# Optimization experiments

Measured on AMD Instinct MI355X. Metric: run time of the kernel, lower is better.

The kernel has to match this reference:

```python
import jax, jax.numpy as jnp
import numpy as np

NUM_HEADS = 32
NUM_KV_HEADS = 8
HEAD_DIM = 128
HIDDEN = 4096
BASE = 10000.0


def setup_inputs() -> dict:
    key = jax.random.key(0)
    ks = jax.random.split(key, 9)
    bs, seq = 1, 2048
    x = jax.random.normal(ks[0], (bs, seq, HIDDEN), dtype=jnp.float32)
    position_ids = jnp.broadcast_to(jnp.arange(seq, dtype=jnp.int32), (bs, seq))
    s = 1.0 / np.sqrt(HIDDEN)
    wq = jax.random.normal(ks[1], (NUM_HEADS * HEAD_DIM, HIDDEN), dtype=jnp.float32) * s
    bq = jnp.zeros((NUM_HEADS * HEAD_DIM,), dtype=jnp.float32)
    wk = jax.random.normal(ks[2], (NUM_KV_HEADS * HEAD_DIM, HIDDEN), dtype=jnp.float32) * s
    bk = jnp.zeros((NUM_KV_HEADS * HEAD_DIM,), dtype=jnp.float32)
    wv = jax.random.normal(ks[3], (NUM_KV_HEADS * HEAD_DIM, HIDDEN), dtype=jnp.float32) * s
    bv = jnp.zeros((NUM_KV_HEADS * HEAD_DIM,), dtype=jnp.float32)
    wo = jax.random.normal(ks[4], (HIDDEN, NUM_HEADS * HEAD_DIM), dtype=jnp.float32) * s
    bo = jnp.zeros((HIDDEN,), dtype=jnp.float32)
    return {"x": x, "position_ids": position_ids, "wq": wq, "bq": bq,
            "wk": wk, "bk": bk, "wv": wv, "bv": bv, "wo": wo, "bo": bo}


def _rotate_half(t):
    h = t.shape[-1] // 2
    return jnp.concatenate([-t[..., h:], t[..., :h]], axis=-1)


def _rope_cos_sin(position_ids, dtype):
    # inv_freq: (head_dim/2,)
    inv_freq = 1.0 / (BASE ** (jnp.arange(0, HEAD_DIM, 2, dtype=jnp.float32) / HEAD_DIM))
    freqs = position_ids.astype(jnp.float32)[..., None] * inv_freq  # (bs, seq, hd/2)
    emb = jnp.concatenate([freqs, freqs], axis=-1)  # (bs, seq, hd)
    return jnp.cos(emb).astype(dtype), jnp.sin(emb).astype(dtype)


def reference(x, position_ids, wq, bq, wk, bk, wv, bv, wo, bo):
    bs, seq, _ = x.shape
    g = NUM_HEADS // NUM_KV_HEADS
    # projections -> (bs, heads, seq, head_dim)
    q = (x @ wq.T + bq).reshape(bs, seq, NUM_HEADS, HEAD_DIM).transpose(0, 2, 1, 3)
    k = (x @ wk.T + bk).reshape(bs, seq, NUM_KV_HEADS, HEAD_DIM).transpose(0, 2, 1, 3)
    v = (x @ wv.T + bv).reshape(bs, seq, NUM_KV_HEADS, HEAD_DIM).transpose(0, 2, 1, 3)
    cos, sin = _rope_cos_sin(position_ids, x.dtype)
    cos, sin = cos[:, None], sin[:, None]  # broadcast over heads
    q = q * cos + _rotate_half(q) * sin
    k = k * cos + _rotate_half(k) * sin
    # grouped attention without expanding kv (same math as repeat_kv)
    qg = q.reshape(bs, NUM_KV_HEADS, g, seq, HEAD_DIM)
    scores = jnp.einsum('bhgqd,bhkd->bhgqk', qg, k) / jnp.sqrt(
        jnp.asarray(HEAD_DIM, dtype=jnp.float32)).astype(x.dtype)
    probs = jax.nn.softmax(scores.astype(jnp.float32), axis=-1).astype(x.dtype)
    out = jnp.einsum('bhgqk,bhkd->bhgqd', probs, v)  # (bs, kvh, g, seq, hd)
    out = out.reshape(bs, NUM_HEADS, seq, HEAD_DIM).transpose(0, 2, 1, 3)
    out = out.reshape(bs, seq, NUM_HEADS * HEAD_DIM)
    return out @ wo.T + bo
```

## Files before the change

kernel.cpp:

```cpp
#include <hip/hip_runtime.h>
#include <stdint.h>

typedef unsigned short u16;
typedef unsigned long long u64;
typedef __attribute__((ext_vector_type(8))) short s8v;
typedef __attribute__((ext_vector_type(4))) float f4v;

#define MFMA(a, b, c) __builtin_amdgcn_mfma_f32_16x16x32_bf16((a), (b), (c), 0, 0, 0)

__device__ __forceinline__ u16 f2b(float f) {
  uint32_t x = __float_as_uint(f);
  x += 0x7fff + ((x >> 16) & 1);
  return (u16)(x >> 16);
}
__device__ __forceinline__ float b2f(u16 u) {
  return __uint_as_float(((uint32_t)u) << 16);
}

__device__ __forceinline__ void gll16(const void* g, void* l) {
  __builtin_amdgcn_global_load_lds((const __attribute__((address_space(1))) uint32_t*)g,
                                   (__attribute__((address_space(3))) uint32_t*)l, 16, 0, 0);
}
__device__ __forceinline__ void bar() { __builtin_amdgcn_s_barrier(); }

__global__ void cvt_kernel(const float* __restrict__ src, u16* __restrict__ dst, int n8) {
  int i = blockIdx.x * 256 + threadIdx.x;
  if (i >= n8) return;
  const float4* s = (const float4*)src;
  float4 f0 = s[2 * (size_t)i], f1 = s[2 * (size_t)i + 1];
  s8v o;
  o[0] = (short)f2b(f0.x); o[1] = (short)f2b(f0.y); o[2] = (short)f2b(f0.z); o[3] = (short)f2b(f0.w);
  o[4] = (short)f2b(f1.x); o[5] = (short)f2b(f1.y); o[6] = (short)f2b(f1.z); o[7] = (short)f2b(f1.w);
  *(s8v*)(dst + 8 * (size_t)i) = o;
}

template <int BM, int MODE>
__global__ __launch_bounds__(512, 2) void gemm8p(
    const u16* __restrict__ A, const u16* __restrict__ W,
    const float* __restrict__ bA, const float* __restrict__ bB, const float* __restrict__ bC,
    float* __restrict__ Cf, u16* __restrict__ Cq, u16* __restrict__ Ck, u16* __restrict__ Cv,
    int Ncols, int K) {
  extern __shared__ u16 smem[];
  constexpr int AO = BM * 64;
  constexpr int BE = 2 * BM * 64;
  constexpr int BO = BE + 16384;
  constexpr int MI = BM / 64;

  const int tid = threadIdx.x;
  const int l = tid & 63, wv = tid >> 6;
  const int wm = wv >> 2, wn = wv & 3;
  const int lr = l & 15, lg = l >> 4;
  const int swz = 16 * (lr & 7);
  const int wrow = wm * (BM / 2);

  const int nwg = gridDim.x;
  int bid = blockIdx.x;
  bid = (bid & 7) * (nwg >> 3) + (bid >> 3);
  const int NB = Ncols >> 8;
  const int m0 = (bid / NB) * BM, n0 = (bid % NB) * 256;

  const size_t K64 = (size_t)64 * K;

  const int sr = tid >> 3;
  const int sc = ((tid & 7) ^ (sr & 7)) * 8;
  const u16* gA = A + (size_t)(m0 + sr) * K + sc;
  const u16* gB = W + (size_t)(n0 + sr) * K + sc;

  auto STA = [&](int P, int h, int kt) {
    const u16* g = gA + (size_t)(h * (BM / 2)) * K + (size_t)kt * 64;
    u16* d = smem + (P ? AO : 0) + h * (BM / 2) * 64 + tid * 8;
    gll16(g, d);
    if constexpr (BM == 256) gll16(g + K64, d + 4096);
  };
  auto STB = [&](int P, int h, int kt) {
    const u16* g = gB + (size_t)(h * 128) * K + (size_t)kt * 64;
    u16* d = smem + (P ? BO : BE) + h * 8192 + tid * 8;
    gll16(g, d);
    gll16(g + K64, d + 4096);
  };

  const char* smc = (const char*)smem;
  s8v a[MI][2], b0[2][2], b1[2][2];
  auto LDA = [&](int P, int QR) {
#pragma unroll
    for (int mi = 0; mi < MI; ++mi)
#pragma unroll
      for (int kk = 0; kk < 2; ++kk)
        a[mi][kk] = *(const s8v*)(smc + (P ? AO * 2 : 0) +
            (wrow + QR * (BM / 4) + mi * 16 + lr) * 128 + ((kk * 64 + lg * 16) ^ swz));
  };
  auto LDB = [&](int P, int QC, s8v bb[2][2]) {
#pragma unroll
    for (int ni = 0; ni < 2; ++ni)
#pragma unroll
      for (int kk = 0; kk < 2; ++kk)
        bb[ni][kk] = *(const s8v*)(smc + (P ? BO * 2 : BE * 2) +
            (wn * 64 + QC * 32 + ni * 16 + lr) * 128 + ((kk * 64 + lg * 16) ^ swz));
  };

  f4v acc[BM / 32][4];
#pragma unroll
  for (int i = 0; i < BM / 32; ++i)
#pragma unroll
    for (int j = 0; j < 4; ++j) acc[i][j] = {0.f, 0.f, 0.f, 0.f};

#define PHMF(QR, QC, B)                                                        \
  __builtin_amdgcn_s_setprio(1);                                               \
  _Pragma("unroll") for (int mi = 0; mi < MI; ++mi)                            \
    _Pragma("unroll") for (int ni = 0; ni < 2; ++ni)                           \
      _Pragma("unroll") for (int kk = 0; kk < 2; ++kk)                         \
        acc[(QR) * MI + mi][(QC) * 2 + ni] =                                   \
            MFMA(a[mi][kk], B[ni][kk], acc[(QR) * MI + mi][(QC) * 2 + ni]);    \
  __builtin_amdgcn_s_setprio(0);

  STB(0, 0, 0); STB(0, 1, 0);
  STA(0, 0, 0); STA(0, 1, 0);
  STB(1, 0, 1); STB(1, 1, 1);
  asm volatile("s_waitcnt vmcnt(4)" ::: "memory");
  bar();

  const int ITERS = K >> 7;
  for (int i = 0; i < ITERS; ++i) {
    const int kn = 2 * i + 2;
    const bool more = (i + 1 < ITERS);
    LDA(0, 0); LDB(0, 0, b0);
    STA(1, 0, 2 * i + 1);
    bar(); PHMF(0, 0, b0); bar();
    LDB(0, 1, b1);
    STA(1, 1, 2 * i + 1);
    bar(); PHMF(0, 1, b1); bar();
    LDA(0, 1);
    if (more) STB(0, 0, kn);
    bar(); PHMF(1, 1, b1); bar();
    if (more) STB(0, 1, kn);
    bar(); PHMF(1, 0, b0);
    asm volatile("s_waitcnt vmcnt(4)" ::: "memory");
    bar();
    LDA(1, 0); LDB(1, 0, b0);
    if (more) STA(0, 0, kn);
    bar(); PHMF(0, 0, b0); bar();
    LDB(1, 1, b1);
    if (more) STA(0, 1, kn);
    bar(); PHMF(0, 1, b1); bar();
    LDA(1, 1);
    if (more) STB(1, 0, 2 * i + 3);
    bar(); PHMF(1, 1, b1); bar();
    if (more) STB(1, 1, 2 * i + 3);
    bar(); PHMF(1, 0, b0);
    asm volatile("s_waitcnt vmcnt(4)" ::: "memory");
    bar();
  }
#undef PHMF

#pragma unroll
  for (int fi = 0; fi < BM / 32; ++fi)
#pragma unroll
    for (int fj = 0; fj < 4; ++fj)
#pragma unroll
      for (int r = 0; r < 4; ++r) {
        int rr = m0 + wrow + fi * 16 + lg * 4 + r;
        int cl = n0 + wn * 64 + fj * 16 + lr;
        float v = acc[fi][fj][r];
        if (MODE == 0) {
          Cf[(size_t)rr * 4096 + cl] = v + bA[cl];
        } else {
          if (cl < 4096)      Cq[(size_t)rr * 4096 + cl] = f2b(v + bA[cl]);
          else if (cl < 5120) Ck[(size_t)rr * 1024 + (cl - 4096)] = f2b(v + bB[cl - 4096]);
          else                Cv[(size_t)(cl - 5120) * 2048 + rr] = f2b(v + bC[cl - 5120]);
        }
      }
}

__global__ void rope_kernel(u16* __restrict__ q, u16* __restrict__ k, const int* __restrict__ pos) {
  int i = blockIdx.x * 256 + threadIdx.x;
  const int NQ = 2048 * 32 * 64;
  const int NK = 2048 * 8 * 64;
  u16* buf;
  int m, d, stride, h;
  if (i < NQ) { buf = q; m = i >> 11; h = (i >> 6) & 31; d = i & 63; stride = 4096; }
  else {
    i -= NQ; if (i >= NK) return;
    buf = k; m = i >> 9; h = (i >> 6) & 7; d = i & 63; stride = 1024;
  }
  size_t base = (size_t)m * stride + h * 128 + d;
  float a = b2f(buf[base]), b = b2f(buf[base + 64]);
  float p = (float)pos[m];
  float ang = p * exp2f(-0.20762050593045952f * (float)d);
  float s, c;
  sincosf(ang, &s, &c);
  buf[base]      = f2b(a * c - b * s);
  buf[base + 64] = f2b(b * c + a * s);
}

__global__ __launch_bounds__(512, 4) void attn_kernel(const u16* __restrict__ Q, const u16* __restrict__ Kb,
                                                      const u16* __restrict__ Vt, u16* __restrict__ Ao) {
  __shared__ __align__(16) u16 Ks[64 * 128];
  __shared__ __align__(16) u16 Vs[128 * 64];
  __shared__ __align__(16) u16 Ps[8 * 16 * 64];
  const int tid = threadIdx.x;
  const int l = tid & 63, wv = tid >> 6;
  const int lr = l & 15, lg = l >> 4;
  const int head = blockIdx.x >> 4, qt = blockIdx.x & 15;
  const int kh = head >> 2;
  const int qrow = qt * 128 + wv * 16 + lr;

  s8v qf[4];
#pragma unroll
  for (int s = 0; s < 4; ++s)
    qf[s] = *(const s8v*)&Q[(size_t)qrow * 4096 + head * 128 + s * 32 + lg * 8];

  f4v zero = {0.f, 0.f, 0.f, 0.f};
  f4v ao[8];
#pragma unroll
  for (int tt = 0; tt < 8; ++tt) ao[tt] = zero;
  float mrun = -1e30f, lrun = 0.f;

  const int ki0 = tid, ki1 = tid + 512;
  const int kr0 = ki0 >> 4, kc0 = (ki0 & 15) ^ (kr0 & 7);
  const int kr1 = ki1 >> 4, kc1 = (ki1 & 15) ^ (kr1 & 7);
  const int vr0 = ki0 >> 3, vc0 = (ki0 & 7) ^ (vr0 & 7);
  const int vr1 = ki1 >> 3, vc1 = (ki1 & 7) ^ (vr1 & 7);
  const u16* Kg = Kb + kh * 128;
  const u16* Vg = Vt + (size_t)(kh * 128) * 2048;
  const u16* kp0 = Kg + (size_t)kr0 * 1024 + kc0 * 8;
  const u16* kp1 = Kg + (size_t)kr1 * 1024 + kc1 * 8;
  const u16* vp0 = Vg + (size_t)vr0 * 2048 + vc0 * 8;
  const u16* vp1 = Vg + (size_t)vr1 * 2048 + vc1 * 8;

  char* KsB = (char*)Ks;
  char* VsB = (char*)Vs;
  char* PwB = (char*)Ps + wv * 2048;
  const int swz = 16 * (lr & 7);
  const float C2 = 0.12753102f;

  for (int t = 0; t < 2048; t += 64) {
    __syncthreads();
    gll16(kp0 + (size_t)t * 1024, KsB + ki0 * 16);
    gll16(kp1 + (size_t)t * 1024, KsB + ki1 * 16);
    gll16(vp0 + t,                VsB + ki0 * 16);
    gll16(vp1 + t,                VsB + ki1 * 16);
    __syncthreads();

    f4v c[4];
#pragma unroll
    for (int j = 0; j < 4; ++j) c[j] = zero;
#pragma unroll
    for (int s = 0; s < 4; ++s) {
#pragma unroll
      for (int j = 0; j < 4; ++j) {
        s8v kf = *(const s8v*)(KsB + (16 * j + lr) * 256 + (((4 * s + lg) * 16) ^ swz));
        c[j] = MFMA(kf, qf[s], c[j]);
      }
    }

    float mx = fmaxf(fmaxf(c[0][0], c[0][1]), fmaxf(c[0][2], c[0][3]));
#pragma unroll
    for (int j = 1; j < 4; ++j)
      mx = fmaxf(mx, fmaxf(fmaxf(c[j][0], c[j][1]), fmaxf(c[j][2], c[j][3])));
    mx = fmaxf(mx, __shfl_xor(mx, 16));
    mx = fmaxf(mx, __shfl_xor(mx, 32));
    float m2x = mx * C2;

    if (!__all(m2x - mrun <= 8.f)) {
      float mnew = fmaxf(mrun, m2x);
      float alpha = __builtin_amdgcn_exp2f(mrun - mnew);
      float ar[4];
#pragma unroll
      for (int r = 0; r < 4; ++r) ar[r] = __shfl(alpha, 4 * lg + r);
#pragma unroll
      for (int tt = 0; tt < 8; ++tt)
#pragma unroll
        for (int r = 0; r < 4; ++r) ao[tt][r] *= ar[r];
      lrun *= alpha;
      mrun = mnew;
    }

    float rs = 0.f;
#pragma unroll
    for (int j = 0; j < 4; ++j) {
      float p0 = __builtin_amdgcn_exp2f(__builtin_fmaf(c[j][0], C2, -mrun));
      float p1 = __builtin_amdgcn_exp2f(__builtin_fmaf(c[j][1], C2, -mrun));
      float p2 = __builtin_amdgcn_exp2f(__builtin_fmaf(c[j][2], C2, -mrun));
      float p3 = __builtin_amdgcn_exp2f(__builtin_fmaf(c[j][3], C2, -mrun));
      rs += (p0 + p1) + (p2 + p3);
      uint32_t lo = (uint32_t)f2b(p0) | ((uint32_t)f2b(p1) << 16);
      uint32_t hi = (uint32_t)f2b(p2) | ((uint32_t)f2b(p3) << 16);
      u64 pak = (u64)lo | ((u64)hi << 32);
      *(u64*)(PwB + lr * 128 + ((32 * j + 8 * lg) ^ swz)) = pak;
    }
    rs += __shfl_xor(rs, 16);
    rs += __shfl_xor(rs, 32);
    lrun += rs;

#pragma unroll
    for (int h = 0; h < 2; ++h) {
      s8v pf = *(const s8v*)(PwB + lr * 128 + ((64 * h + 16 * lg) ^ swz));
#pragma unroll
      for (int tt = 0; tt < 8; ++tt) {
        s8v vf = *(const s8v*)(VsB + (16 * tt + lr) * 128 + (((4 * h + lg) * 16) ^ swz));
        ao[tt] = MFMA(pf, vf, ao[tt]);
      }
    }
  }

  float inv = 1.f / lrun;
  float ir[4];
#pragma unroll
  for (int r = 0; r < 4; ++r) ir[r] = __shfl(inv, 4 * lg + r);
#pragma unroll
  for (int tt = 0; tt < 8; ++tt)
#pragma unroll
    for (int r = 0; r < 4; ++r)
      Ao[(size_t)(qt * 128 + wv * 16 + 4 * lg + r) * 4096 + head * 128 + 16 * tt + lr] =
          f2b(ao[tt][r] * ir[r]);
}

extern "C" void kernel_launch(void* const* d_in, const int* in_sizes, int n_in,
                              void* d_out, int out_size, void* d_ws, size_t ws_size,
                              hipStream_t stream) {
  const float* x  = (const float*)d_in[0];
  const int*   pos = (const int*)d_in[1];
  const float* wq = (const float*)d_in[2];
  const float* bq = (const float*)d_in[3];
  const float* wk = (const float*)d_in[4];
  const float* bk = (const float*)d_in[5];
  const float* wv = (const float*)d_in[6];
  const float* bv = (const float*)d_in[7];
  const float* wo = (const float*)d_in[8];
  const float* bo = (const float*)d_in[9];
  float* out = (float*)d_out;

  char* ws = (char*)d_ws;
  u16* xb   = (u16*)(ws + 0);
  u16* wqkv = (u16*)(ws + 16777216);
  u16* wob  = (u16*)(ws + 67108864);
  u16* qb   = (u16*)(ws + 100663296);
  u16* kb   = (u16*)(ws + 117440512);
  u16* vT   = (u16*)(ws + 121634816);
  u16* ab   = (u16*)(ws + 125829120);

  auto cv = [&](const float* s, u16* d, size_t n) {
    int n8 = (int)(n / 8);
    cvt_kernel<<<(n8 + 255) / 256, 256, 0, stream>>>(s, d, n8);
  };
  cv(x,  xb,   (size_t)2048 * 4096);
  cv(wq, wqkv, (size_t)4096 * 4096);
  cv(wk, wqkv + (size_t)4096 * 4096, (size_t)1024 * 4096);
  cv(wv, wqkv + (size_t)5120 * 4096, (size_t)1024 * 4096);
  cv(wo, wob,  (size_t)4096 * 4096);

  gemm8p<256, 2><<<192, 512, 131072, stream>>>(xb, wqkv, bq, bk, bv,
                                               nullptr, qb, kb, vT, 6144, 4096);
  rope_kernel<<<(2048 * 32 * 64 + 2048 * 8 * 64) / 256, 256, 0, stream>>>(qb, kb, pos);
  attn_kernel<<<512, 512, 0, stream>>>(qb, kb, vT, ab);
  gemm8p<128, 0><<<256, 512, 98304, stream>>>(ab, wob, bo, nullptr, nullptr,
                                              out, nullptr, nullptr, nullptr, 4096, 4096);
}
```

Baseline: 366.8 us.

## Swap GEMM operands to compute transposed outputs with LDS-staged coalesced stores

Both GEMMs now treat the weights as the M operand and the activations as the N operand, so each tile computes the transposed output (features by tokens). The epilogue stages accumulators through per-wave LDS buffers and writes each token's feature span with wide vector stores instead of scattered 2-byte or 4-byte stores. The V output is now naturally token-contiguous for the transposed layout. This aims to cut epilogue store inefficiency, at the cost of an extra barrier, LDS round-trips and hardcoded problem dimensions such as NB=8.

```diff
diff --git a/kernel.cpp b/kernel.cpp
--- a/kernel.cpp
+++ b/kernel.cpp
@@ -36,10 +36,10 @@
 
 template <int BM, int MODE>
 __global__ __launch_bounds__(512, 2) void gemm8p(
-    const u16* __restrict__ A, const u16* __restrict__ W,
+    const u16* __restrict__ A, const u16* __restrict__ Bact,
     const float* __restrict__ bA, const float* __restrict__ bB, const float* __restrict__ bC,
     float* __restrict__ Cf, u16* __restrict__ Cq, u16* __restrict__ Ck, u16* __restrict__ Cv,
-    int Ncols, int K) {
+    int K) {
   extern __shared__ u16 smem[];
   constexpr int AO = BM * 64;
   constexpr int BE = 2 * BM * 64;
@@ -56,7 +56,7 @@
   const int nwg = gridDim.x;
   int bid = blockIdx.x;
   bid = (bid & 7) * (nwg >> 3) + (bid >> 3);
-  const int NB = Ncols >> 8;
+  const int NB = 8;
   const int m0 = (bid / NB) * BM, n0 = (bid % NB) * 256;
 
   const size_t K64 = (size_t)64 * K;
@@ -64,7 +64,7 @@
   const int sr = tid >> 3;
   const int sc = ((tid & 7) ^ (sr & 7)) * 8;
   const u16* gA = A + (size_t)(m0 + sr) * K + sc;
-  const u16* gB = W + (size_t)(n0 + sr) * K + sc;
+  const u16* gB = Bact + (size_t)(n0 + sr) * K + sc;
 
   auto STA = [&](int P, int h, int kt) {
     const u16* g = gA + (size_t)(h * (BM / 2)) * K + (size_t)kt * 64;
@@ -152,23 +152,73 @@
   }
 #undef PHMF
 
-#pragma unroll
-  for (int fi = 0; fi < BM / 32; ++fi)
-#pragma unroll
-    for (int fj = 0; fj < 4; ++fj)
-#pragma unroll
-      for (int r = 0; r < 4; ++r) {
-        int rr = m0 + wrow + fi * 16 + lg * 4 + r;
-        int cl = n0 + wn * 64 + fj * 16 + lr;
-        float v = acc[fi][fj][r];
-        if (MODE == 0) {
-          Cf[(size_t)rr * 4096 + cl] = v + bA[cl];
-        } else {
-          if (cl < 4096)      Cq[(size_t)rr * 4096 + cl] = f2b(v + bA[cl]);
-          else if (cl < 5120) Ck[(size_t)rr * 1024 + (cl - 4096)] = f2b(v + bB[cl - 4096]);
-          else                Cv[(size_t)(cl - 5120) * 2048 + rr] = f2b(v + bC[cl - 5120]);
+  bar();
+
+  if (MODE == 2) {
+    const int mt = m0 >> 8;
+    if (mt < 20) {
+      u16* dst; int fstride, fbase; const float* bias;
+      if (mt < 16) { dst = Cq; fstride = 4096; fbase = m0;        bias = bA; }
+      else         { dst = Ck; fstride = 1024; fbase = m0 - 4096; bias = bB; }
+      u16* buf = smem + wv * 4352;
+#pragma unroll
+      for (int c = 0; c < 2; ++c) {
+#pragma unroll
+        for (int fj2 = 0; fj2 < 2; ++fj2) {
+          const int fj = 2 * c + fj2;
+          const int tl = fj2 * 16 + lr;
+#pragma unroll
+          for (int fi = 0; fi < BM / 32; ++fi)
+#pragma unroll
+            for (int r = 0; r < 4; ++r) {
+              const int fl = fi * 16 + lg * 4 + r;
+              buf[tl * 136 + fl] = f2b(acc[fi][fj][r] + bias[fbase + wrow + fl]);
+            }
         }
+        asm volatile("s_waitcnt lgkmcnt(0)" ::: "memory");
+        const int row = l >> 1, half = l & 1;
+        const int tok = n0 + wn * 64 + c * 32 + row;
+        const u16* src = buf + row * 136 + half * 64;
+        u16* g = dst + (size_t)tok * fstride + fbase + wrow + half * 64;
+#pragma unroll
+        for (int i = 0; i < 8; ++i)
+          *(s8v*)(g + i * 8) = *(const s8v*)(src + i * 8);
+        asm volatile("s_waitcnt lgkmcnt(0)" ::: "memory");
       }
+    } else {
+#pragma unroll
+      for (int fi = 0; fi < BM / 32; ++fi)
+#pragma unroll
+        for (int fj = 0; fj < 4; ++fj)
+#pragma unroll
+          for (int r = 0; r < 4; ++r) {
+            const int feat = m0 - 5120 + wrow + fi * 16 + lg * 4 + r;
+            const int tok = n0 + wn * 64 + fj * 16 + lr;
+            Cv[(size_t)feat * 2048 + tok] = f2b(acc[fi][fj][r] + bC[feat]);
+          }
+    }
+  } else {
+    float* buf = (float*)smem + wv * 1088;
+#pragma unroll
+    for (int c = 0; c < 4; ++c) {
+#pragma unroll
+      for (int fi = 0; fi < BM / 32; ++fi)
+#pragma unroll
+        for (int r = 0; r < 4; ++r) {
+          const int fl = fi * 16 + lg * 4 + r;
+          buf[lr * 68 + fl] = acc[fi][c][r] + bA[m0 + wrow + fl];
+        }
+      asm volatile("s_waitcnt lgkmcnt(0)" ::: "memory");
+      const int row = l >> 2, q4 = l & 3;
+      const int tok = n0 + wn * 64 + c * 16 + row;
+      float* g = Cf + (size_t)tok * 4096 + m0 + wrow + q4 * 16;
+      const float* src = buf + row * 68 + q4 * 16;
+#pragma unroll
+      for (int i = 0; i < 4; ++i)
+        *(f4v*)(g + i * 4) = *(const f4v*)(src + i * 4);
+      asm volatile("s_waitcnt lgkmcnt(0)" ::: "memory");
+    }
+  }
 }
 
 __global__ void rope_kernel(u16* __restrict__ q, u16* __restrict__ k, const int* __restrict__ pos) {
@@ -349,10 +399,10 @@
   cv(wv, wqkv + (size_t)5120 * 4096, (size_t)1024 * 4096);
   cv(wo, wob,  (size_t)4096 * 4096);
 
-  gemm8p<256, 2><<<192, 512, 131072, stream>>>(xb, wqkv, bq, bk, bv,
-                                               nullptr, qb, kb, vT, 6144, 4096);
+  gemm8p<256, 2><<<192, 512, 131072, stream>>>(wqkv, xb, bq, bk, bv,
+                                               nullptr, qb, kb, vT, 4096);
   rope_kernel<<<(2048 * 32 * 64 + 2048 * 8 * 64) / 256, 256, 0, stream>>>(qb, kb, pos);
   attn_kernel<<<512, 512, 0, stream>>>(qb, kb, vT, ab);
-  gemm8p<128, 0><<<256, 512, 98304, stream>>>(ab, wob, bo, nullptr, nullptr,
-                                              out, nullptr, nullptr, nullptr, 4096, 4096);
-}
+  gemm8p<128, 0><<<256, 512, 98304, stream>>>(wob, ab, bo, nullptr, nullptr,
+                                              out, nullptr, nullptr, nullptr, 4096);
+}
```

Result: faster. 347.0 us (-5.4%).
